# Kernel optimization log

Hardware: AMD Instinct MI355X
Metric: run time of the kernel (lower is better)

## Reference

```python
import math
import jax, jax.numpy as jnp
import numpy as np

B, Q, K, D = 32, 1024, 1024, 128
MASK_VALUE = -1000000.0


def setup_inputs() -> dict:
    key = jax.random.key(0)
    kq, kk, kv, kl = jax.random.split(key, 4)
    return {
        "queries": jax.random.normal(kq, (B, Q, D), dtype=jnp.float32),
        "keys": jax.random.normal(kk, (B, K, D), dtype=jnp.float32),
        "values": jax.random.normal(kv, (B, K, D), dtype=jnp.float32),
        "valid_lens": jax.random.randint(kl, (B,), 1, K + 1, dtype=jnp.int32),
    }


def reference(queries, keys, values, valid_lens):
    d = queries.shape[-1]
    # scores: [B, Q, K]
    scores = jnp.einsum("bqd,bkd->bqk", queries, keys) / math.sqrt(d)
    # key-padding mask: position k valid iff k < valid_lens[b] (broadcast over queries)
    mask = jnp.arange(keys.shape[1])[None, None, :] < valid_lens[:, None, None]
    scores = jnp.where(mask, scores, MASK_VALUE)
    attn = jax.nn.softmax(scores, axis=-1)
    # dropout p=0.0 -> identity
    return jnp.einsum("bqk,bkv->bqv", attn, values)
```

## Files before the change

kernel.cpp:

```cpp
#include <hip/hip_runtime.h>
#include <math.h>

typedef _Float16 f16;
typedef __attribute__((ext_vector_type(8))) _Float16 f16x8;
typedef __attribute__((ext_vector_type(4))) _Float16 f16x4;
typedef __attribute__((ext_vector_type(4))) float f32x4;

constexpr int BATCH = 32;
constexpr int QL = 1024;
constexpr int KL = 1024;
constexpr int D = 128;
constexpr int BQ = 64;
constexpr int BK = 64;
constexpr int DKP = 136;
constexpr int BKP = 72;

#define CSC 0.12752863187087177f

static __device__ __forceinline__ f16x4 pk4(float x, float y, float z, float w) {
  auto a = __builtin_amdgcn_cvt_pkrtz(x, y);
  auto b = __builtin_amdgcn_cvt_pkrtz(z, w);
  f16x4 h;
  h[0] = (f16)a[0]; h[1] = (f16)a[1]; h[2] = (f16)b[0]; h[3] = (f16)b[1];
  return h;
}
static __device__ __forceinline__ f16x8 pk8(float4 u, float4 v) {
  f16x4 a = pk4(u.x, u.y, u.z, u.w);
  f16x4 b = pk4(v.x, v.y, v.z, v.w);
  f16x8 h;
  h[0] = a[0]; h[1] = a[1]; h[2] = a[2]; h[3] = a[3];
  h[4] = b[0]; h[5] = b[1]; h[6] = b[2]; h[7] = b[3];
  return h;
}

template <int CTRL>
static __device__ __forceinline__ float dppf(float v) {
  int x = __float_as_int(v);
  x = __builtin_amdgcn_update_dpp(x, x, CTRL, 0xf, 0xf, false);
  return __int_as_float(x);
}
static __device__ __forceinline__ float rmax16(float v) {
  v = fmaxf(v, dppf<0xB1>(v));
  v = fmaxf(v, dppf<0x4E>(v));
  v = fmaxf(v, dppf<0x141>(v));
  v = fmaxf(v, dppf<0x140>(v));
  return v;
}
static __device__ __forceinline__ float rsum16(float v) {
  v += dppf<0xB1>(v);
  v += dppf<0x4E>(v);
  v += dppf<0x141>(v);
  v += dppf<0x140>(v);
  return v;
}

#define ISSUE(KR, VR, T)                                                   \
  do {                                                                     \
    const float4* Kt = (const float4*)(Kb + (size_t)(T) * BK * D);         \
    _Pragma("unroll")                                                      \
    for (int i_ = 0; i_ < 4; ++i_) {                                       \
      int cc_ = tid + i_ * 256;                                            \
      int row_ = cc_ >> 4, d04_ = (cc_ & 15) * 2;                          \
      KR[2 * i_]     = Kt[row_ * 32 + d04_];                               \
      KR[2 * i_ + 1] = Kt[row_ * 32 + d04_ + 1];                           \
    }                                                                      \
    const float* Vt = Vb + (size_t)(T) * BK * D;                           \
    _Pragma("unroll")                                                      \
    for (int i_ = 0; i_ < 2; ++i_) {                                       \
      int f_ = tid + i_ * 256;                                             \
      const float* base_ = Vt + (size_t)((f_ & 15) * 4) * D + (f_ >> 4) * 4; \
      VR[i_ * 4 + 0] = *(const float4*)(base_);                            \
      VR[i_ * 4 + 1] = *(const float4*)(base_ + D);                        \
      VR[i_ * 4 + 2] = *(const float4*)(base_ + 2 * D);                    \
      VR[i_ * 4 + 3] = *(const float4*)(base_ + 3 * D);                    \
    }                                                                      \
  } while (0)

#define DRAIN(KR, VR, NB)                                                  \
  do {                                                                     \
    _Pragma("unroll")                                                      \
    for (int i_ = 0; i_ < 4; ++i_) {                                       \
      int cc_ = tid + i_ * 256;                                            \
      int row_ = cc_ >> 4, d0_ = (cc_ & 15) * 8;                           \
      int rp_ = (row_ & 3) * 16 + (row_ >> 2);                             \
      *(f16x8*)&sK[NB][rp_][d0_] = pk8(KR[2 * i_], KR[2 * i_ + 1]);        \
    }                                                                      \
    _Pragma("unroll")                                                      \
    for (int i_ = 0; i_ < 2; ++i_) {                                       \
      int f_ = tid + i_ * 256;                                             \
      int k0_ = (f_ & 15) * 4, d0_ = (f_ >> 4) * 4;                        \
      float4 r0_ = VR[i_*4+0], r1_ = VR[i_*4+1], r2_ = VR[i_*4+2], r3_ = VR[i_*4+3]; \
      *(f16x4*)&sVT[NB][d0_ + 0][k0_] = pk4(r0_.x, r1_.x, r2_.x, r3_.x);   \
      *(f16x4*)&sVT[NB][d0_ + 1][k0_] = pk4(r0_.y, r1_.y, r2_.y, r3_.y);   \
      *(f16x4*)&sVT[NB][d0_ + 2][k0_] = pk4(r0_.z, r1_.z, r2_.z, r3_.z);   \
      *(f16x4*)&sVT[NB][d0_ + 3][k0_] = pk4(r0_.w, r1_.w, r2_.w, r3_.w);   \
    }                                                                      \
  } while (0)

#define TILE_BARRIER()                                                     \
  do {                                                                     \
    asm volatile("s_waitcnt lgkmcnt(0)" ::: "memory");                     \
    __builtin_amdgcn_s_barrier();                                          \
    asm volatile("" ::: "memory");                                         \
  } while (0)

#define COMPUTE(CB)                                                        \
  do {                                                                     \
    f32x4 sv[4];                                                           \
    _Pragma("unroll")                                                      \
    for (int ct = 0; ct < 4; ++ct) {                                       \
      f32x4 cacc = (f32x4){0.f, 0.f, 0.f, 0.f};                            \
      _Pragma("unroll")                                                    \
      for (int kc = 0; kc < 4; ++kc) {                                     \
        f16x8 kf = *(const f16x8*)&sK[CB][ct * 16 + l16][kc * 32 + quad * 8]; \
        cacc = __builtin_amdgcn_mfma_f32_16x16x32_f16(qfrag[kc], kf, cacc, 0, 0, 0); \
      }                                                                    \
      sv[ct] = cacc;                                                       \
    }                                                                      \
     \
    _Pragma("unroll")                                                      \
    for (int ct = 0; ct < 4; ++ct) {                                       \
      bool ok = (t * BK + l16 * 4 + ct) < vl;                              \
      _Pragma("unroll")                                                    \
      for (int r = 0; r < 4; ++r)                                          \
        sv[ct][r] = ok ? sv[ct][r] * CSC : -1.0e9f;                        \
    }                                                                      \
                  \
    float mnew[4], alpha[4];                                               \
    _Pragma("unroll")                                                      \
    for (int r = 0; r < 4; ++r) {                                          \
      float v = fmaxf(fmaxf(sv[0][r], sv[1][r]), fmaxf(sv[2][r], sv[3][r])); \
      v = rmax16(v);                                                       \
      mnew[r]  = fmaxf(m2[r], v);                                          \
      alpha[r] = __builtin_amdgcn_exp2f(m2[r] - mnew[r]);                  \
      m2[r]    = mnew[r];                                                  \
    }                                                                      \
    _Pragma("unroll")                                                      \
    for (int r = 0; r < 4; ++r) {                                          \
      float ls = 0.f;                                                      \
      _Pragma("unroll")                                                    \
      for (int ct = 0; ct < 4; ++ct) {                                     \
        float p = __builtin_amdgcn_exp2f(sv[ct][r] - mnew[r]);             \
        sv[ct][r] = p;                                                     \
        ls += p;                                                           \
      }                                                                    \
      lsum[r] = lsum[r] * alpha[r] + rsum16(ls);                           \
      *(f16x4*)&sP[wave][quad * 4 + r][l16 * 4] =                          \
          pk4(sv[0][r], sv[1][r], sv[2][r], sv[3][r]);                     \
      _Pragma("unroll")                                                    \
      for (int dt = 0; dt < 8; ++dt) o[dt][r] *= alpha[r];                 \
    }                                                                      \
           \
    asm volatile("s_waitcnt lgkmcnt(0)" ::: "memory");                     \
    _Pragma("unroll")                                                      \
    for (int ks = 0; ks < 2; ++ks) {                                       \
      f16x8 pf = *(const f16x8*)&sP[wave][l16][ks * 32 + quad * 8];        \
      _Pragma("unroll")                                                    \
      for (int dt = 0; dt < 8; ++dt) {                                     \
        f16x8 vf = *(const f16x8*)&sVT[CB][dt * 16 + l16][ks * 32 + quad * 8]; \
        o[dt] = __builtin_amdgcn_mfma_f32_16x16x32_f16(pf, vf, o[dt], 0, 0, 0); \
      }                                                                    \
    }                                                                      \
  } while (0)

__global__ __launch_bounds__(256, 2)
void attn_fwd(const float* __restrict__ Qp, const float* __restrict__ Kp,
              const float* __restrict__ Vp, const int* __restrict__ VLp,
              float* __restrict__ Op) {
  __shared__ f16 sK[2][BK][DKP];
  __shared__ f16 sVT[2][D][BKP];
  __shared__ f16 sP[4][16][BKP];
  __shared__ int sN[32];
  __shared__ int sI[32];

  const int tid  = threadIdx.x;
  const int wave = tid >> 6, lane = tid & 63;
  const int l16  = lane & 15, quad = lane >> 4;

  if (tid < 32) sN[tid] = (VLp[tid] + BK - 1) / BK;
  __syncthreads();
  if (tid < 32) {
    int nb = sN[tid], r = 0;
    #pragma unroll
    for (int k = 0; k < 32; ++k) {
      int nk = sN[k];
      r += (nk > nb) || (nk == nb && k < tid);
    }
    sI[r] = tid;
  }
  __syncthreads();
  const int xcd = blockIdx.x & 7;
  const int j   = (int)blockIdx.x >> 3;
  const int jj  = (j < 32) ? j : (95 - j);
  const int lr  = jj >> 4;
  const int qt  = jj & 15;
  const int grank = (lr == 0) ? xcd : (lr == 1) ? (15 - xcd)
                  : (lr == 2) ? (16 + xcd) : (31 - xcd);
  const int b  = sI[grank];
  const int vl = VLp[b];

  const float* Kb = Kp + (size_t)b * KL * D;
  const float* Vb = Vp + (size_t)b * KL * D;
  const int ntiles = (vl + BK - 1) / BK;

  float4 kA[8], vA[8], kB[8], vB[8];

  const float* Qb = Qp + ((size_t)(b * QL + qt * BQ + wave * 16 + l16)) * D;
  float4 qtmp[8];
  #pragma unroll
  for (int kc = 0; kc < 4; ++kc) {
    const float* p = Qb + kc * 32 + quad * 8;
    qtmp[2 * kc]     = *(const float4*)p;
    qtmp[2 * kc + 1] = *(const float4*)(p + 4);
  }

  ISSUE(kA, vA, 0);
  if (ntiles > 1) ISSUE(kB, vB, 1);

  f16x8 qfrag[4];
  #pragma unroll
  for (int kc = 0; kc < 4; ++kc) qfrag[kc] = pk8(qtmp[2 * kc], qtmp[2 * kc + 1]);

  float m2[4]   = {-INFINITY, -INFINITY, -INFINITY, -INFINITY};
  float lsum[4] = {0.f, 0.f, 0.f, 0.f};
  f32x4 o[8];
  #pragma unroll
  for (int dt = 0; dt < 8; ++dt) o[dt] = (f32x4){0.f, 0.f, 0.f, 0.f};

  DRAIN(kA, vA, 0);
  TILE_BARRIER();

  int t = 0;
  for (;;) {
    if (t + 2 < ntiles) ISSUE(kA, vA, t + 2);
    COMPUTE(0);
    if (t + 1 >= ntiles) break;
    DRAIN(kB, vB, 1);
    TILE_BARRIER();
    ++t;
    if (t + 2 < ntiles) ISSUE(kB, vB, t + 2);
    COMPUTE(1);
    if (t + 1 >= ntiles) break;
    DRAIN(kA, vA, 0);
    TILE_BARRIER();
    ++t;
  }

  float* Ob = Op + ((size_t)(b * QL + qt * BQ + wave * 16)) * D;
  #pragma unroll
  for (int r = 0; r < 4; ++r) {
    float inv = 1.0f / lsum[r];
    int row = quad * 4 + r;
    #pragma unroll
    for (int dt = 0; dt < 8; ++dt)
      Ob[(size_t)row * D + dt * 16 + l16] = o[dt][r] * inv;
  }
}

extern "C" void kernel_launch(void* const* d_in, const int* in_sizes, int n_in,
                              void* d_out, int out_size, void* d_ws, size_t ws_size,
                              hipStream_t stream) {
  const float* Qp = (const float*)d_in[0];
  const float* Kp = (const float*)d_in[1];
  const float* Vp = (const float*)d_in[2];
  const int*   VL = (const int*)d_in[3];
  float* Op = (float*)d_out;

  attn_fwd<<<dim3(QL / BQ * BATCH), dim3(256), 0, stream>>>(Qp, Kp, Vp, VL, Op);
}
```

Before: 127.9 us.

## Compute transposed S so P stays in registers; double query tile per block

Each wave now owns 32 query rows (two 16-row halves), so every K/V tile loaded into shared memory serves twice as many queries. The score MFMA is transposed (K as A operand), which lets the softmax output P be packed directly into registers as the B operand of the PV MFMA and removes the sP shared-memory round trip and DPP reductions in favor of cross-quad shuffles. The softmax scale is folded into Q at load time, masking runs only on the tail tile, and output is written with float4 stores. Register prefetch drops from two tiles ahead to one and occupancy is lowered to one block per SIMD group, while the grid shrinks to half as many blocks, which risks latency hiding and load balance.

```diff
diff --git a/kernel.cpp b/kernel.cpp
--- a/kernel.cpp
+++ b/kernel.cpp
@@ -10,7 +10,7 @@
 constexpr int QL = 1024;
 constexpr int KL = 1024;
 constexpr int D = 128;
-constexpr int BQ = 64;
+constexpr int BQ = 128;
 constexpr int BK = 64;
 constexpr int DKP = 136;
 constexpr int BKP = 72;
@@ -32,26 +32,24 @@
   h[4] = b[0]; h[5] = b[1]; h[6] = b[2]; h[7] = b[3];
   return h;
 }
-
-template <int CTRL>
-static __device__ __forceinline__ float dppf(float v) {
-  int x = __float_as_int(v);
-  x = __builtin_amdgcn_update_dpp(x, x, CTRL, 0xf, 0xf, false);
-  return __int_as_float(x);
-}
-static __device__ __forceinline__ float rmax16(float v) {
-  v = fmaxf(v, dppf<0xB1>(v));
-  v = fmaxf(v, dppf<0x4E>(v));
-  v = fmaxf(v, dppf<0x141>(v));
-  v = fmaxf(v, dppf<0x140>(v));
-  return v;
-}
-static __device__ __forceinline__ float rsum16(float v) {
-  v += dppf<0xB1>(v);
-  v += dppf<0x4E>(v);
-  v += dppf<0x141>(v);
-  v += dppf<0x140>(v);
-  return v;
+static __device__ __forceinline__ f16x8 pk8v(f32x4 a, f32x4 b) {
+  auto x0 = __builtin_amdgcn_cvt_pkrtz(a[0], a[1]);
+  auto x1 = __builtin_amdgcn_cvt_pkrtz(a[2], a[3]);
+  auto x2 = __builtin_amdgcn_cvt_pkrtz(b[0], b[1]);
+  auto x3 = __builtin_amdgcn_cvt_pkrtz(b[2], b[3]);
+  f16x8 h;
+  h[0] = x0[0]; h[1] = x0[1]; h[2] = x1[0]; h[3] = x1[1];
+  h[4] = x2[0]; h[5] = x2[1]; h[6] = x3[0]; h[7] = x3[1];
+  return h;
+}
+static __device__ __forceinline__ f16x8 pk8s(float4 u, float4 v) {
+  float4 a = {u.x * CSC, u.y * CSC, u.z * CSC, u.w * CSC};
+  float4 b = {v.x * CSC, v.y * CSC, v.z * CSC, v.w * CSC};
+  return pk8(a, b);
+}
+
+static __device__ __forceinline__ int krp(int kk) {
+  return ((kk >> 5) << 5) | (((kk >> 2) & 1) << 4) | (((kk >> 3) & 3) << 2) | (kk & 3);
 }
 
 #define ISSUE(KR, VR, T)                                                   \
@@ -82,8 +80,7 @@
     for (int i_ = 0; i_ < 4; ++i_) {                                       \
       int cc_ = tid + i_ * 256;                                            \
       int row_ = cc_ >> 4, d0_ = (cc_ & 15) * 8;                           \
-      int rp_ = (row_ & 3) * 16 + (row_ >> 2);                             \
-      *(f16x8*)&sK[NB][rp_][d0_] = pk8(KR[2 * i_], KR[2 * i_ + 1]);        \
+      *(f16x8*)&sK[NB][krp(row_)][d0_] = pk8(KR[2 * i_], KR[2 * i_ + 1]);  \
     }                                                                      \
     _Pragma("unroll")                                                      \
     for (int i_ = 0; i_ < 2; ++i_) {                                       \
@@ -104,72 +101,43 @@
     asm volatile("" ::: "memory");                                         \
   } while (0)
 
-#define COMPUTE(CB)                                                        \
-  do {                                                                     \
-    f32x4 sv[4];                                                           \
-    _Pragma("unroll")                                                      \
-    for (int ct = 0; ct < 4; ++ct) {                                       \
-      f32x4 cacc = (f32x4){0.f, 0.f, 0.f, 0.f};                            \
+#define SOFTMAX_HALF(SV, MM, LL, PF, OO)                                   \
+  do {                                                                     \
+    float t0_ = fmaxf(fmaxf(SV[0][0], SV[0][1]), fmaxf(SV[0][2], SV[0][3]));\
+    float t1_ = fmaxf(fmaxf(SV[1][0], SV[1][1]), fmaxf(SV[1][2], SV[1][3]));\
+    float t2_ = fmaxf(fmaxf(SV[2][0], SV[2][1]), fmaxf(SV[2][2], SV[2][3]));\
+    float t3_ = fmaxf(fmaxf(SV[3][0], SV[3][1]), fmaxf(SV[3][2], SV[3][3]));\
+    float pmax_ = fmaxf(fmaxf(t0_, t1_), fmaxf(t2_, t3_));                 \
+    pmax_ = fmaxf(pmax_, __shfl_xor(pmax_, 16));                           \
+    pmax_ = fmaxf(pmax_, __shfl_xor(pmax_, 32));                           \
+    float mnew_  = fmaxf(MM, pmax_);                                       \
+    float alpha_ = __builtin_amdgcn_exp2f(MM - mnew_);                     \
+    MM = mnew_;                                                            \
+    float ls_ = 0.f;                                                       \
+    _Pragma("unroll")                                                      \
+    for (int ct_ = 0; ct_ < 4; ++ct_) {                                    \
       _Pragma("unroll")                                                    \
-      for (int kc = 0; kc < 4; ++kc) {                                     \
-        f16x8 kf = *(const f16x8*)&sK[CB][ct * 16 + l16][kc * 32 + quad * 8]; \
-        cacc = __builtin_amdgcn_mfma_f32_16x16x32_f16(qfrag[kc], kf, cacc, 0, 0, 0); \
+      for (int r_ = 0; r_ < 4; ++r_) {                                     \
+        float p_ = __builtin_amdgcn_exp2f(SV[ct_][r_] - mnew_);            \
+        SV[ct_][r_] = p_;                                                  \
+        ls_ += p_;                                                         \
       }                                                                    \
-      sv[ct] = cacc;                                                       \
-    }                                                                      \
-     \
-    _Pragma("unroll")                                                      \
-    for (int ct = 0; ct < 4; ++ct) {                                       \
-      bool ok = (t * BK + l16 * 4 + ct) < vl;                              \
-      _Pragma("unroll")                                                    \
-      for (int r = 0; r < 4; ++r)                                          \
-        sv[ct][r] = ok ? sv[ct][r] * CSC : -1.0e9f;                        \
-    }                                                                      \
-                  \
-    float mnew[4], alpha[4];                                               \
-    _Pragma("unroll")                                                      \
-    for (int r = 0; r < 4; ++r) {                                          \
-      float v = fmaxf(fmaxf(sv[0][r], sv[1][r]), fmaxf(sv[2][r], sv[3][r])); \
-      v = rmax16(v);                                                       \
-      mnew[r]  = fmaxf(m2[r], v);                                          \
-      alpha[r] = __builtin_amdgcn_exp2f(m2[r] - mnew[r]);                  \
-      m2[r]    = mnew[r];                                                  \
-    }                                                                      \
-    _Pragma("unroll")                                                      \
-    for (int r = 0; r < 4; ++r) {                                          \
-      float ls = 0.f;                                                      \
-      _Pragma("unroll")                                                    \
-      for (int ct = 0; ct < 4; ++ct) {                                     \
-        float p = __builtin_amdgcn_exp2f(sv[ct][r] - mnew[r]);             \
-        sv[ct][r] = p;                                                     \
-        ls += p;                                                           \
-      }                                                                    \
-      lsum[r] = lsum[r] * alpha[r] + rsum16(ls);                           \
-      *(f16x4*)&sP[wave][quad * 4 + r][l16 * 4] =                          \
-          pk4(sv[0][r], sv[1][r], sv[2][r], sv[3][r]);                     \
-      _Pragma("unroll")                                                    \
-      for (int dt = 0; dt < 8; ++dt) o[dt][r] *= alpha[r];                 \
-    }                                                                      \
-           \
-    asm volatile("s_waitcnt lgkmcnt(0)" ::: "memory");                     \
-    _Pragma("unroll")                                                      \
-    for (int ks = 0; ks < 2; ++ks) {                                       \
-      f16x8 pf = *(const f16x8*)&sP[wave][l16][ks * 32 + quad * 8];        \
-      _Pragma("unroll")                                                    \
-      for (int dt = 0; dt < 8; ++dt) {                                     \
-        f16x8 vf = *(const f16x8*)&sVT[CB][dt * 16 + l16][ks * 32 + quad * 8]; \
-        o[dt] = __builtin_amdgcn_mfma_f32_16x16x32_f16(pf, vf, o[dt], 0, 0, 0); \
-      }                                                                    \
-    }                                                                      \
-  } while (0)
-
-__global__ __launch_bounds__(256, 2)
+    }                                                                      \
+    ls_ += __shfl_xor(ls_, 16);                                            \
+    ls_ += __shfl_xor(ls_, 32);                                            \
+    LL = LL * alpha_ + ls_;                                                \
+    PF[0] = pk8v(SV[0], SV[1]);                                            \
+    PF[1] = pk8v(SV[2], SV[3]);                                            \
+    _Pragma("unroll")                                                      \
+    for (int dt_ = 0; dt_ < 8; ++dt_) OO[dt_] *= alpha_;                   \
+  } while (0)
+
+__global__ __launch_bounds__(256, 1)
 void attn_fwd(const float* __restrict__ Qp, const float* __restrict__ Kp,
               const float* __restrict__ Vp, const int* __restrict__ VLp,
               float* __restrict__ Op) {
   __shared__ f16 sK[2][BK][DKP];
   __shared__ f16 sVT[2][D][BKP];
-  __shared__ f16 sP[4][16][BKP];
   __shared__ int sN[32];
   __shared__ int sI[32];
 
@@ -191,9 +159,8 @@
   __syncthreads();
   const int xcd = blockIdx.x & 7;
   const int j   = (int)blockIdx.x >> 3;
-  const int jj  = (j < 32) ? j : (95 - j);
-  const int lr  = jj >> 4;
-  const int qt  = jj & 15;
+  const int lr  = j >> 3;
+  const int qt  = j & 7;
   const int grank = (lr == 0) ? xcd : (lr == 1) ? (15 - xcd)
                   : (lr == 2) ? (16 + xcd) : (31 - xcd);
   const int b  = sI[grank];
@@ -203,57 +170,99 @@
   const float* Vb = Vp + (size_t)b * KL * D;
   const int ntiles = (vl + BK - 1) / BK;
 
-  float4 kA[8], vA[8], kB[8], vB[8];
-
-  const float* Qb = Qp + ((size_t)(b * QL + qt * BQ + wave * 16 + l16)) * D;
-  float4 qtmp[8];
-  #pragma unroll
-  for (int kc = 0; kc < 4; ++kc) {
-    const float* p = Qb + kc * 32 + quad * 8;
-    qtmp[2 * kc]     = *(const float4*)p;
-    qtmp[2 * kc + 1] = *(const float4*)(p + 4);
-  }
-
-  ISSUE(kA, vA, 0);
-  if (ntiles > 1) ISSUE(kB, vB, 1);
-
-  f16x8 qfrag[4];
-  #pragma unroll
-  for (int kc = 0; kc < 4; ++kc) qfrag[kc] = pk8(qtmp[2 * kc], qtmp[2 * kc + 1]);
-
-  float m2[4]   = {-INFINITY, -INFINITY, -INFINITY, -INFINITY};
-  float lsum[4] = {0.f, 0.f, 0.f, 0.f};
-  f32x4 o[8];
-  #pragma unroll
-  for (int dt = 0; dt < 8; ++dt) o[dt] = (f32x4){0.f, 0.f, 0.f, 0.f};
-
-  DRAIN(kA, vA, 0);
+  float4 kreg[8], vreg[8];
+
+  const float* Qb = Qp + ((size_t)(b * QL + qt * BQ + wave * 32 + l16)) * D;
+  float4 qtmp[16];
+  #pragma unroll
+  for (int h = 0; h < 2; ++h)
+    #pragma unroll
+    for (int kc = 0; kc < 4; ++kc) {
+      const float* p = Qb + h * 16 * D + kc * 32 + quad * 8;
+      qtmp[h * 8 + 2 * kc]     = *(const float4*)p;
+      qtmp[h * 8 + 2 * kc + 1] = *(const float4*)(p + 4);
+    }
+
+  ISSUE(kreg, vreg, 0);
+
+  f16x8 qf0[4], qf1[4];
+  #pragma unroll
+  for (int kc = 0; kc < 4; ++kc)
+    qf0[kc] = pk8s(qtmp[2 * kc], qtmp[2 * kc + 1]);
+  #pragma unroll
+  for (int kc = 0; kc < 4; ++kc)
+    qf1[kc] = pk8s(qtmp[8 + 2 * kc], qtmp[8 + 2 * kc + 1]);
+
+  float m0 = -INFINITY, m1 = -INFINITY;
+  float l0 = 0.f, l1 = 0.f;
+  f32x4 o0[8], o1[8];
+  #pragma unroll
+  for (int dt = 0; dt < 8; ++dt) {
+    o0[dt] = (f32x4){0.f, 0.f, 0.f, 0.f};
+    o1[dt] = (f32x4){0.f, 0.f, 0.f, 0.f};
+  }
+
+  DRAIN(kreg, vreg, 0);
   TILE_BARRIER();
 
-  int t = 0;
-  for (;;) {
-    if (t + 2 < ntiles) ISSUE(kA, vA, t + 2);
-    COMPUTE(0);
-    if (t + 1 >= ntiles) break;
-    DRAIN(kB, vB, 1);
+  for (int t = 0; t < ntiles; ++t) {
+    const int cur = t & 1, nxt = cur ^ 1;
+    const bool more = (t + 1 < ntiles);
+
+    if (more) ISSUE(kreg, vreg, t + 1);
+
+    f32x4 s0[4], s1[4];
+    #pragma unroll
+    for (int ct = 0; ct < 4; ++ct) {
+      s0[ct] = (f32x4){0.f, 0.f, 0.f, 0.f};
+      s1[ct] = (f32x4){0.f, 0.f, 0.f, 0.f};
+      #pragma unroll
+      for (int kc = 0; kc < 4; ++kc) {
+        f16x8 kf = *(const f16x8*)&sK[cur][ct * 16 + l16][kc * 32 + quad * 8];
+        s0[ct] = __builtin_amdgcn_mfma_f32_16x16x32_f16(kf, qf0[kc], s0[ct], 0, 0, 0);
+        s1[ct] = __builtin_amdgcn_mfma_f32_16x16x32_f16(kf, qf1[kc], s1[ct], 0, 0, 0);
+      }
+    }
+
+    if (t * BK + BK > vl) {
+      #pragma unroll
+      for (int ct = 0; ct < 4; ++ct) {
+        int kb = t * BK + (ct >> 1) * 32 + (ct & 1) * 4 + quad * 8;
+        #pragma unroll
+        for (int r = 0; r < 4; ++r) {
+          bool ok = (kb + r) < vl;
+          s0[ct][r] = ok ? s0[ct][r] : -1.0e9f;
+          s1[ct][r] = ok ? s1[ct][r] : -1.0e9f;
+        }
+      }
+    }
+
+    f16x8 pf0[2], pf1[2];
+    SOFTMAX_HALF(s0, m0, l0, pf0, o0);
+    SOFTMAX_HALF(s1, m1, l1, pf1, o1);
+
+    #pragma unroll
+    for (int ks = 0; ks < 2; ++ks) {
+      #pragma unroll
+      for (int dt = 0; dt < 8; ++dt) {
+        f16x8 vf = *(const f16x8*)&sVT[cur][dt * 16 + l16][ks * 32 + quad * 8];
+        o0[dt] = __builtin_amdgcn_mfma_f32_16x16x32_f16(vf, pf0[ks], o0[dt], 0, 0, 0);
+        o1[dt] = __builtin_amdgcn_mfma_f32_16x16x32_f16(vf, pf1[ks], o1[dt], 0, 0, 0);
+      }
+    }
+
+    if (more) DRAIN(kreg, vreg, nxt);
     TILE_BARRIER();
-    ++t;
-    if (t + 2 < ntiles) ISSUE(kB, vB, t + 2);
-    COMPUTE(1);
-    if (t + 1 >= ntiles) break;
-    DRAIN(kA, vA, 0);
-    TILE_BARRIER();
-    ++t;
-  }
-
-  float* Ob = Op + ((size_t)(b * QL + qt * BQ + wave * 16)) * D;
-  #pragma unroll
-  for (int r = 0; r < 4; ++r) {
-    float inv = 1.0f / lsum[r];
-    int row = quad * 4 + r;
-    #pragma unroll
-    for (int dt = 0; dt < 8; ++dt)
-      Ob[(size_t)row * D + dt * 16 + l16] = o[dt][r] * inv;
+  }
+
+  float* Ob = Op + ((size_t)(b * QL + qt * BQ + wave * 32)) * D;
+  const float inv0 = 1.0f / l0, inv1 = 1.0f / l1;
+  #pragma unroll
+  for (int dt = 0; dt < 8; ++dt) {
+    float4 w0 = {o0[dt][0] * inv0, o0[dt][1] * inv0, o0[dt][2] * inv0, o0[dt][3] * inv0};
+    float4 w1 = {o1[dt][0] * inv1, o1[dt][1] * inv1, o1[dt][2] * inv1, o1[dt][3] * inv1};
+    *(float4*)&Ob[(size_t)l16 * D + dt * 16 + quad * 4]        = w0;
+    *(float4*)&Ob[(size_t)(16 + l16) * D + dt * 16 + quad * 4] = w1;
   }
 }
 
```

Result: no change. 126.7 us (-1.0%).
